# Kernel optimization log

Hardware: AMD Instinct MI355X
Metric: run time of the kernel (lower is better)

The kernel has to match this reference:

```python
import jax, jax.numpy as jnp
import numpy as np

EPS = 1e-8  # torch F.cosine_similarity eps


def setup_inputs() -> dict:
    key = jax.random.key(0)
    ks = jax.random.split(key, 5)
    S, Q, D_in, D, N_WAY, K_SHOT = 100, 4096, 21168, 64, 20, 5
    return {
        "support_images": jax.random.normal(ks[0], (S, D_in), dtype=jnp.float32),
        "support_labels": jax.random.randint(ks[1], (S,), 0, N_WAY),
        "query_images": jax.random.normal(ks[2], (Q, D_in), dtype=jnp.float32),
        "n_way": N_WAY,
        "k_shot": K_SHOT,
        "backbone_w": jax.random.normal(ks[3], (D_in, D), dtype=jnp.float32) * 0.02,
        "backbone_b": jax.random.normal(ks[4], (D,), dtype=jnp.float32) * 0.02,
    }


def _l2_normalize(x):
    # matches torch cosine_similarity: x / max(||x||, eps)
    n = jnp.maximum(jnp.linalg.norm(x, axis=-1, keepdims=True), EPS)
    return x / n


def reference(support_images, support_labels, query_images, n_way, k_shot,
              backbone_w, backbone_b):
    # Backbone: linear embedding (stand-in for conv feature extractor)
    support_emb = support_images @ backbone_w + backbone_b   # [S, D]
    query_emb = query_images @ backbone_w + backbone_b       # [Q, D]

    # Cosine similarity between every query and every support sample: [Q, S]
    sims = _l2_normalize(query_emb) @ _l2_normalize(support_emb).T

    # Softmax over the support axis (per query), as in the original loop
    attn = jax.nn.softmax(sims, axis=1)                      # [Q, S]

    # Per-label scatter-add == one-hot segment-sum: [Q, n_way]
    one_hot = jax.nn.one_hot(support_labels, n_way, dtype=attn.dtype)  # [S, n_way]
    logits = attn @ one_hot
    return logits
```

## Files before the change

kernel.cpp:

```cpp
#include <hip/hip_runtime.h>
#include <hip/hip_bf16.h>
#include <math.h>

#define DEMB 64
#define BM   64
#define KSMAX 32

using short8 = __attribute__((ext_vector_type(8))) short;
using u16x8  = __attribute__((ext_vector_type(8))) unsigned short;
using f32x4  = __attribute__((ext_vector_type(4))) float;

__device__ __forceinline__ unsigned short f2bf(float x) {
    union { float f; unsigned u; } v; v.f = x;
    unsigned r = v.u + 0x7fffu + ((v.u >> 16) & 1u);
    return (unsigned short)(r >> 16);
}

__global__ __launch_bounds__(256) void prep_wt(
    const float* __restrict__ W, unsigned short* __restrict__ Wt,
    int Din, int Wstride)
{
    __shared__ unsigned short tile[64][65];
    const int k0 = blockIdx.x * 64;
    const int tid = threadIdx.x;
    #pragma unroll
    for (int i = 0; i < 16; ++i) {
        int kk = i * 4 + (tid >> 6);
        int c  = tid & 63;
        int k  = k0 + kk;
        float x = (k < Din) ? W[(size_t)k * DEMB + c] : 0.f;
        tile[kk][c] = f2bf(x);
    }
    __syncthreads();
    #pragma unroll
    for (int i = 0; i < 16; ++i) {
        int c  = i * 4 + (tid >> 6);
        int kk = tid & 63;
        Wt[(size_t)c * Wstride + k0 + kk] = tile[kk][c];
    }
}

__global__ __launch_bounds__(256) void gemm_mfma(
    const float* __restrict__ Xq, const float* __restrict__ Xs,
    const unsigned short* __restrict__ Wt,
    float* __restrict__ qpart, float* __restrict__ spart,
    int Q, int S, int Din, int Wstride, int nQb, int cpk, int nchunk)
{
    __shared__ unsigned short As[2][BM * 32];
    __shared__ unsigned short Ws[2][64 * 32];

    const int tid  = threadIdx.x;
    const int wave = tid >> 6;
    const int lane = tid & 63;
    const int kg   = blockIdx.y;

    const bool isS = (int)blockIdx.x >= nQb;
    const float* X = isS ? Xs : Xq;
    const int nrows = isS ? S : Q;
    const int r0 = (isS ? ((int)blockIdx.x - nQb) : (int)blockIdx.x) * BM;
    float* part = isS ? spart : qpart;
    const int prow = isS ? 128 : Q;

    const int arow = tid >> 2;
    const int ak   = (tid & 3) * 8;
    const bool aval = (r0 + arow) < nrows;
    const float* aptr = X + (size_t)(r0 + arow) * Din;
    const unsigned short* wptr = Wt + (size_t)(tid >> 2) * Wstride + (tid & 3) * 8;

    const int col16 = lane & 15;
    const int frow  = 16 * wave + col16;
    const int fk    = (lane >> 4) * 8;

    f32x4 acc[4] = { {0.f,0.f,0.f,0.f}, {0.f,0.f,0.f,0.f},
                     {0.f,0.f,0.f,0.f}, {0.f,0.f,0.f,0.f} };

    const int c0 = kg * cpk;
    int c1 = c0 + cpk; if (c1 > nchunk) c1 = nchunk;

    {
        const int k0 = c0 * 32;
        const int kk = k0 + ak;
        float4 a0 = {}, a1 = {};
        if (aval && kk + 8 <= Din) {
            a0 = *reinterpret_cast<const float4*>(aptr + kk);
            a1 = *reinterpret_cast<const float4*>(aptr + kk + 4);
        }
        u16x8 wv = *reinterpret_cast<const u16x8*>(wptr + k0);
        u16x8 ap = { f2bf(a0.x), f2bf(a0.y), f2bf(a0.z), f2bf(a0.w),
                     f2bf(a1.x), f2bf(a1.y), f2bf(a1.z), f2bf(a1.w) };
        *reinterpret_cast<u16x8*>(&As[0][arow * 32 + ak]) = ap;
        *reinterpret_cast<u16x8*>(&Ws[0][tid * 8]) = wv;
        __syncthreads();
    }

    int cur = 0;
    for (int c = c0; c < c1; ++c) {
        const int cn = c + 1;
        const bool pf = (cn < c1);
        float4 a0 = {}, a1 = {};
        u16x8 wv = {0,0,0,0,0,0,0,0};
        if (pf) {
            const int k0 = cn * 32;
            const int kk = k0 + ak;
            if (aval && kk + 8 <= Din) {
                a0 = *reinterpret_cast<const float4*>(aptr + kk);
                a1 = *reinterpret_cast<const float4*>(aptr + kk + 4);
            }
            wv = *reinterpret_cast<const u16x8*>(wptr + k0);
        }

        short8 af = *reinterpret_cast<const short8*>(&As[cur][frow * 32 + fk]);
        #pragma unroll
        for (int cb = 0; cb < 4; ++cb) {
            short8 bf = *reinterpret_cast<const short8*>(
                &Ws[cur][(16 * cb + col16) * 32 + fk]);
            acc[cb] = __builtin_amdgcn_mfma_f32_16x16x32_bf16(af, bf, acc[cb], 0, 0, 0);
        }

        if (pf) {
            u16x8 ap = { f2bf(a0.x), f2bf(a0.y), f2bf(a0.z), f2bf(a0.w),
                         f2bf(a1.x), f2bf(a1.y), f2bf(a1.z), f2bf(a1.w) };
            *reinterpret_cast<u16x8*>(&As[cur ^ 1][arow * 32 + ak]) = ap;
            *reinterpret_cast<u16x8*>(&Ws[cur ^ 1][tid * 8]) = wv;
        }
        __syncthreads();
        cur ^= 1;
    }

    #pragma unroll
    for (int cb = 0; cb < 4; ++cb) {
        #pragma unroll
        for (int i = 0; i < 4; ++i) {
            int row = r0 + 16 * wave + (lane >> 4) * 4 + i;
            if (row < nrows)
                part[((size_t)kg * prow + row) * DEMB + 16 * cb + col16] = acc[cb][i];
        }
    }
}

__global__ void support_finalize(const float* __restrict__ spart,
                                 const float* __restrict__ bias,
                                 float* __restrict__ sn, int S, int nkg)
{
    int s = blockIdx.x;
    int c = threadIdx.x;
    float e = bias[c];
    for (int g = 0; g < nkg; ++g)
        e += spart[((size_t)g * 128 + s) * DEMB + c];
    float ss = e * e;
    #pragma unroll
    for (int o = 32; o >= 1; o >>= 1) ss += __shfl_xor(ss, o, 64);
    sn[(size_t)s * DEMB + c] = e / fmaxf(sqrtf(ss), 1e-8f);
}

__global__ __launch_bounds__(256) void attend(
    const float* __restrict__ qpart, const float* __restrict__ sn_g,
    const float* __restrict__ bias, const int* __restrict__ labels,
    const int* __restrict__ p_nway, float* __restrict__ out,
    int S, int Q, int nkg)
{
    __shared__ float sn[100][65];
    __shared__ float qn[4][64];
    __shared__ float bins[4][32];
    __shared__ int   lab[100];

    const int tid  = threadIdx.x;
    const int w    = tid >> 6;
    const int lane = tid & 63;
    const int nw   = *p_nway;

    for (int i = tid; i < S * DEMB; i += 256) sn[i >> 6][i & 63] = sn_g[i];
    if (tid < S) lab[tid] = labels[tid];

    const int q = blockIdx.x * 4 + w;

    float e = bias[lane];
    for (int g = 0; g < nkg; ++g)
        e += qpart[((size_t)g * Q + q) * DEMB + lane];
    float ss = e * e;
    #pragma unroll
    for (int o = 32; o >= 1; o >>= 1) ss += __shfl_xor(ss, o, 64);
    e /= fmaxf(sqrtf(ss), 1e-8f);
    qn[w][lane] = e;
    if (lane < 32) bins[w][lane] = 0.f;
    __syncthreads();

    const bool v1 = (lane + 64) < S;
    const int  s1 = v1 ? lane + 64 : 0;
    float sim0 = 0.f, sim1 = 0.f;
    #pragma unroll 8
    for (int c = 0; c < DEMB; ++c) {
        float qc = qn[w][c];
        sim0 += qc * sn[lane][c];
        sim1 += qc * sn[s1][c];
    }
    if (!v1) sim1 = -INFINITY;

    float lm = fmaxf(sim0, sim1);
    #pragma unroll
    for (int o = 32; o >= 1; o >>= 1) lm = fmaxf(lm, __shfl_xor(lm, o, 64));
    float e0 = __expf(sim0 - lm);
    float e1 = v1 ? __expf(sim1 - lm) : 0.f;
    float d = e0 + e1;
    #pragma unroll
    for (int o = 32; o >= 1; o >>= 1) d += __shfl_xor(d, o, 64);

    atomicAdd(&bins[w][lab[lane]], e0);
    if (v1) atomicAdd(&bins[w][lab[s1]], e1);
    __syncthreads();

    if (lane < nw) out[(size_t)q * nw + lane] = bins[w][lane] / d;
}

extern "C" void kernel_launch(void* const* d_in, const int* in_sizes, int n_in,
                              void* d_out, int out_size, void* d_ws, size_t ws_size,
                              hipStream_t stream)
{
    const float* sup    = (const float*)d_in[0];
    const int*   labels = (const int*)d_in[1];
    const float* qry    = (const float*)d_in[2];
    const int*   p_nway = (const int*)d_in[3];
    const float* W      = (const float*)d_in[5];
    const float* bias   = (const float*)d_in[6];
    float* out = (float*)d_out;

    const int D   = DEMB;
    const int Din = in_sizes[5] / D;
    const int Q   = in_sizes[2] / Din;
    const int S   = in_sizes[1];

    const int nchunk  = (Din + 31) / 32;
    const int Wstride = nchunk * 32;

    char* wsb = (char*)d_ws;
    size_t wt_bytes = (size_t)64 * Wstride * sizeof(unsigned short);
    wt_bytes = (wt_bytes + 255) & ~(size_t)255;
    size_t sn_bytes = (size_t)S * D * sizeof(float);
    sn_bytes = (sn_bytes + 255) & ~(size_t)255;
    size_t per_ks = ((size_t)Q * D + 128 * D) * sizeof(float);

    size_t fixed = wt_bytes + sn_bytes;
    int ks = 1;
    if (ws_size > fixed + per_ks) {
        size_t avail = (ws_size - fixed) / per_ks;
        ks = (int)(avail < KSMAX ? avail : KSMAX);
        if (ks < 1) ks = 1;
    }
    const int cpk = (nchunk + ks - 1) / ks;
    const int nkg = (nchunk + cpk - 1) / cpk;

    unsigned short* Wt = (unsigned short*)wsb;
    float* sn    = (float*)(wsb + wt_bytes);
    float* spart = (float*)(wsb + wt_bytes + sn_bytes);
    float* qpart = spart + (size_t)nkg * 128 * D;

    hipLaunchKernelGGL(prep_wt, dim3((Din + 63) / 64), dim3(256), 0, stream,
                       W, Wt, Din, Wstride);

    const int nQb = (Q + BM - 1) / BM;
    const int nSb = (S + BM - 1) / BM;
    hipLaunchKernelGGL(gemm_mfma, dim3(nQb + nSb, nkg), dim3(256), 0, stream,
                       qry, sup, Wt, qpart, spart, Q, S, Din, Wstride, nQb, cpk, nchunk);

    hipLaunchKernelGGL(support_finalize, dim3(S), dim3(64), 0, stream,
                       spart, bias, sn, S, nkg);

    hipLaunchKernelGGL(attend, dim3(Q / 4), dim3(256), 0, stream,
                       qpart, sn, bias, labels, p_nway, out, S, Q, nkg);
}
```

Measured before the change: 137.0 us.

## Load bf16 W fragments directly into registers and pad A tile in LDS

Removes the shared-memory staging of the transposed weight tile. Each wave now loads its MFMA B fragments straight from global memory into registers, double-buffered across two unrolled iterations. Pads the A tile row stride from 32 to 40 elements to reduce LDS bank conflicts on fragment reads. The aim is less LDS traffic and lower store-to-read latency, at the cost of redundant global W loads across the four waves, which should mostly hit cache.

```diff
diff --git a/kernel.cpp b/kernel.cpp
--- a/kernel.cpp
+++ b/kernel.cpp
@@ -5,6 +5,7 @@
 #define DEMB 64
 #define BM   64
 #define KSMAX 32
+#define APAD 40
 
 using short8 = __attribute__((ext_vector_type(8))) short;
 using u16x8  = __attribute__((ext_vector_type(8))) unsigned short;
@@ -46,8 +47,7 @@
     float* __restrict__ qpart, float* __restrict__ spart,
     int Q, int S, int Din, int Wstride, int nQb, int cpk, int nchunk)
 {
-    __shared__ unsigned short As[2][BM * 32];
-    __shared__ unsigned short Ws[2][64 * 32];
+    __shared__ unsigned short As[2][BM * APAD];
 
     const int tid  = threadIdx.x;
     const int wave = tid >> 6;
@@ -65,11 +65,11 @@
     const int ak   = (tid & 3) * 8;
     const bool aval = (r0 + arow) < nrows;
     const float* aptr = X + (size_t)(r0 + arow) * Din;
-    const unsigned short* wptr = Wt + (size_t)(tid >> 2) * Wstride + (tid & 3) * 8;
 
     const int col16 = lane & 15;
     const int frow  = 16 * wave + col16;
     const int fk    = (lane >> 4) * 8;
+    const unsigned short* bptr = Wt + (size_t)col16 * Wstride + fk;
 
     f32x4 acc[4] = { {0.f,0.f,0.f,0.f}, {0.f,0.f,0.f,0.f},
                      {0.f,0.f,0.f,0.f}, {0.f,0.f,0.f,0.f} };
@@ -77,55 +77,74 @@
     const int c0 = kg * cpk;
     int c1 = c0 + cpk; if (c1 > nchunk) c1 = nchunk;
 
-    {
-        const int k0 = c0 * 32;
-        const int kk = k0 + ak;
-        float4 a0 = {}, a1 = {};
-        if (aval && kk + 8 <= Din) {
-            a0 = *reinterpret_cast<const float4*>(aptr + kk);
-            a1 = *reinterpret_cast<const float4*>(aptr + kk + 4);
+#define LOADA(c, A0, A1) do {                                                  \
+    const int k0_ = (c) * 32;                                                  \
+    const int kk_ = k0_ + ak;                                                  \
+    if (aval && kk_ + 8 <= Din) {                                              \
+        A0 = *reinterpret_cast<const float4*>(aptr + kk_);                     \
+        A1 = *reinterpret_cast<const float4*>(aptr + kk_ + 4);                 \
+    } else {                                                                   \
+        A0 = make_float4(0.f,0.f,0.f,0.f); A1 = make_float4(0.f,0.f,0.f,0.f);  \
+    }                                                                          \
+} while (0)
+
+#define LOADB(c, BV) do {                                                      \
+    const int k0_ = (c) * 32;                                                  \
+    BV[0] = *reinterpret_cast<const u16x8*>(bptr + k0_);                       \
+    BV[1] = *reinterpret_cast<const u16x8*>(bptr + (size_t)16 * Wstride + k0_);\
+    BV[2] = *reinterpret_cast<const u16x8*>(bptr + (size_t)32 * Wstride + k0_);\
+    BV[3] = *reinterpret_cast<const u16x8*>(bptr + (size_t)48 * Wstride + k0_);\
+} while (0)
+
+#define WRITEA(P, A0, A1) do {                                                 \
+    u16x8 ap_ = { f2bf(A0.x), f2bf(A0.y), f2bf(A0.z), f2bf(A0.w),              \
+                  f2bf(A1.x), f2bf(A1.y), f2bf(A1.z), f2bf(A1.w) };            \
+    *reinterpret_cast<u16x8*>(&As[P][arow * APAD + ak]) = ap_;                 \
+} while (0)
+
+#define COMPUTE(P, BV) do {                                                    \
+    short8 af_ = *reinterpret_cast<const short8*>(&As[P][frow * APAD + fk]);   \
+    acc[0] = __builtin_amdgcn_mfma_f32_16x16x32_bf16(af_, (short8)BV[0], acc[0], 0, 0, 0); \
+    acc[1] = __builtin_amdgcn_mfma_f32_16x16x32_bf16(af_, (short8)BV[1], acc[1], 0, 0, 0); \
+    acc[2] = __builtin_amdgcn_mfma_f32_16x16x32_bf16(af_, (short8)BV[2], acc[2], 0, 0, 0); \
+    acc[3] = __builtin_amdgcn_mfma_f32_16x16x32_bf16(af_, (short8)BV[3], acc[3], 0, 0, 0); \
+} while (0)
+
+    float4 a0, a1;
+    u16x8 bA[4], bB[4];
+
+    LOADA(c0, a0, a1);
+    LOADB(c0, bA);
+    WRITEA(0, a0, a1);
+    __syncthreads();
+
+    int c = c0, cur = 0;
+    while (c < c1) {
+        {
+            const int cn = c + 1;
+            const bool pf = cn < c1;
+            if (pf) { LOADA(cn, a0, a1); LOADB(cn, bB); }
+            COMPUTE(cur, bA);
+            if (pf) WRITEA(cur ^ 1, a0, a1);
+            __syncthreads();
+            cur ^= 1; ++c;
         }
-        u16x8 wv = *reinterpret_cast<const u16x8*>(wptr + k0);
-        u16x8 ap = { f2bf(a0.x), f2bf(a0.y), f2bf(a0.z), f2bf(a0.w),
-                     f2bf(a1.x), f2bf(a1.y), f2bf(a1.z), f2bf(a1.w) };
-        *reinterpret_cast<u16x8*>(&As[0][arow * 32 + ak]) = ap;
-        *reinterpret_cast<u16x8*>(&Ws[0][tid * 8]) = wv;
-        __syncthreads();
-    }
-
-    int cur = 0;
-    for (int c = c0; c < c1; ++c) {
-        const int cn = c + 1;
-        const bool pf = (cn < c1);
-        float4 a0 = {}, a1 = {};
-        u16x8 wv = {0,0,0,0,0,0,0,0};
-        if (pf) {
-            const int k0 = cn * 32;
-            const int kk = k0 + ak;
-            if (aval && kk + 8 <= Din) {
-                a0 = *reinterpret_cast<const float4*>(aptr + kk);
-                a1 = *reinterpret_cast<const float4*>(aptr + kk + 4);
-            }
-            wv = *reinterpret_cast<const u16x8*>(wptr + k0);
+        if (c >= c1) break;
+        {
+            const int cn = c + 1;
+            const bool pf = cn < c1;
+            if (pf) { LOADA(cn, a0, a1); LOADB(cn, bA); }
+            COMPUTE(cur, bB);
+            if (pf) WRITEA(cur ^ 1, a0, a1);
+            __syncthreads();
+            cur ^= 1; ++c;
         }
-
-        short8 af = *reinterpret_cast<const short8*>(&As[cur][frow * 32 + fk]);
-        #pragma unroll
-        for (int cb = 0; cb < 4; ++cb) {
-            short8 bf = *reinterpret_cast<const short8*>(
-                &Ws[cur][(16 * cb + col16) * 32 + fk]);
-            acc[cb] = __builtin_amdgcn_mfma_f32_16x16x32_bf16(af, bf, acc[cb], 0, 0, 0);
-        }
-
-        if (pf) {
-            u16x8 ap = { f2bf(a0.x), f2bf(a0.y), f2bf(a0.z), f2bf(a0.w),
-                         f2bf(a1.x), f2bf(a1.y), f2bf(a1.z), f2bf(a1.w) };
-            *reinterpret_cast<u16x8*>(&As[cur ^ 1][arow * 32 + ak]) = ap;
-            *reinterpret_cast<u16x8*>(&Ws[cur ^ 1][tid * 8]) = wv;
-        }
-        __syncthreads();
-        cur ^= 1;
-    }
+    }
+
+#undef LOADA
+#undef LOADB
+#undef WRITEA
+#undef COMPUTE
 
     #pragma unroll
     for (int cb = 0; cb < 4; ++cb) {
```

Result: slower. 162.4 us (+18.6%).
